# Optimization experiments

Measured on AMD Instinct MI355X. Metric: run time of the kernel, lower is better.

## Reference

```python
import jax, jax.numpy as jnp
import numpy as np

B, S, D, H = 4, 1024, 1024, 16
HD = D // H
EPS = 1e-5


def _layernorm(x, g, b):
    m = jnp.mean(x, axis=-1, keepdims=True)
    v = jnp.mean((x - m) ** 2, axis=-1, keepdims=True)
    return (x - m) * jax.lax.rsqrt(v + EPS) * g + b


def setup_inputs() -> dict:
    key = jax.random.key(0)
    ks = jax.random.split(key, 8)
    sc = 1.0 / np.sqrt(D)
    return {
        "x": jax.random.normal(ks[0], (B, S, D), dtype=jnp.float32),
        "seq_len": jax.random.randint(ks[1], (B,), 1, S + 1, dtype=jnp.int32),
        "Wq": jax.random.normal(ks[2], (D, D), dtype=jnp.float32) * sc,
        "bq": jnp.zeros((D,), dtype=jnp.float32),
        "Wk": jax.random.normal(ks[3], (D, D), dtype=jnp.float32) * sc,
        "bk": jnp.zeros((D,), dtype=jnp.float32),
        "Wv": jax.random.normal(ks[4], (D, D), dtype=jnp.float32) * sc,
        "bv": jnp.zeros((D,), dtype=jnp.float32),
        "ln_g": jnp.ones((HD,), dtype=jnp.float32),
        "ln_b": jnp.zeros((HD,), dtype=jnp.float32),
    }


def reference(x, seq_len, Wq, bq, Wk, bk, Wv, bv, ln_g, ln_b):
    # Faithful quirk: k and v are projections of the ALREADY projected q.
    q = x @ Wq.T + bq                      # [B,S,D]
    k = q @ Wk.T + bk
    v = q @ Wv.T + bv
    # [B,S,D] -> [B,H,S,HD]
    def split_heads(t):
        return t.reshape(B, S, H, HD).transpose(0, 2, 1, 3)
    q, k, v = split_heads(q), split_heads(k), split_heads(v)
    # shared per-head LayerNorm over head_dim
    q = _layernorm(q, ln_g, ln_b)
    k = _layernorm(k, ln_g, ln_b)
    v = _layernorm(v, ln_g, ln_b)
    # raw scores (no temperature scaling in the original; temperature=1.0 unused)
    scores = jnp.einsum("bhqd,bhkd->bhqk", q, k)
    # encoder_mask: multiplicative validity mask on key positions, repeated per head
    mask = (jnp.arange(S)[None, :] < seq_len[:, None]).astype(scores.dtype)  # [B,S]
    scores = scores * mask[:, None, None, :]
    attn = jax.nn.softmax(scores, axis=-1)
    # dropout is identity at inference
    out = jnp.einsum("bhqk,bhkd->bhqd", attn, v)
    return out.transpose(0, 2, 1, 3).reshape(B, S, D)
```

## Files before the change

### kernel.cpp

```cpp
#include <hip/hip_runtime.h>

#define B_  4
#define S_  1024
#define D_  1024
#define H_  16
#define HD_ 64
#define EPS_ 1e-5f

typedef _Float16 f16x8 __attribute__((ext_vector_type(8)));
typedef _Float16 f16x4 __attribute__((ext_vector_type(4)));
typedef __bf16 bf16x8 __attribute__((ext_vector_type(8)));
typedef float  f32x4  __attribute__((ext_vector_type(4)));
typedef unsigned short ushort8v __attribute__((ext_vector_type(8)));

static __device__ __forceinline__ unsigned short f2bf(float f) {
  union { float f; unsigned u; } v; v.f = f;
  unsigned r = v.u + 0x7fffu + ((v.u >> 16) & 1u);
  return (unsigned short)(r >> 16);
}
static __device__ __forceinline__ float bf2f(unsigned short u) {
  union { unsigned u; float f; } v; v.u = ((unsigned)u) << 16;
  return v.f;
}

#define GLD16(gp, lp) __builtin_amdgcn_global_load_lds( \
    (const __attribute__((address_space(1))) void*)(gp), \
    (__attribute__((address_space(3))) void*)(lp), 16, 0, 0)

__global__ __launch_bounds__(256) void cvt_all(
    const float* __restrict__ x,  _Float16* __restrict__ xh,
    const float* __restrict__ Wq, _Float16* __restrict__ wqh,
    const float* __restrict__ Wk, _Float16* __restrict__ wkh,
    const float* __restrict__ Wv, _Float16* __restrict__ wvh) {
  int bid = blockIdx.x;
  const float* src; _Float16* dst; int base;
  if (bid < 4096)      { src = x;  dst = xh;  base = bid; }
  else if (bid < 5120) { src = Wq; dst = wqh; base = bid - 4096; }
  else if (bid < 6144) { src = Wk; dst = wkh; base = bid - 5120; }
  else                 { src = Wv; dst = wvh; base = bid - 6144; }
  int i = base * 1024 + threadIdx.x * 4;
  float4 f = *(const float4*)(src + i);
  f16x4 h;
  h.x = (_Float16)f.x; h.y = (_Float16)f.y; h.z = (_Float16)f.z; h.w = (_Float16)f.w;
  *(f16x4*)(dst + i) = h;
}

__global__ __launch_bounds__(256, 2) void gemm_bt_bias(
    const _Float16* __restrict__ A,
    const _Float16* __restrict__ B0, const float* __restrict__ bias0,
    _Float16* __restrict__ C0,
    const _Float16* __restrict__ B1, const float* __restrict__ bias1,
    _Float16* __restrict__ C1,
    int M, int N, int K)
{
  const _Float16* Bm = blockIdx.z ? B1 : B0;
  const float* bias  = blockIdx.z ? bias1 : bias0;
  _Float16* C        = blockIdx.z ? C1 : C0;

  __shared__ _Float16 As[128 * 32];
  __shared__ _Float16 Bs[64 * 32];

  int tid  = threadIdx.x;
  int lane = tid & 63;
  int wave = tid >> 6;
  int wm = wave >> 1, wn = wave & 1;
  int qd = lane >> 4, l15 = lane & 15;

  long row0 = (long)blockIdx.y * 128;
  long col0 = (long)blockIdx.x * 64;

  int r_a = tid >> 2;
  int c_a = (tid & 3) * 8;

  f32x4 acc[4][2] = {};

  for (int kk = 0; kk < K; kk += 32) {
    GLD16(A  + (row0 + r_a) * K + kk + c_a,      As + tid * 8);
    GLD16(A  + (row0 + 64 + r_a) * K + kk + c_a, As + 2048 + tid * 8);
    GLD16(Bm + (col0 + r_a) * K + kk + c_a,      Bs + tid * 8);
    __syncthreads();

    f16x8 af[4], bfr[2];
    for (int t = 0; t < 4; t++)
      af[t]  = *(const f16x8*)(As + (wm * 64 + t * 16 + l15) * 32 + qd * 8);
    for (int j = 0; j < 2; j++)
      bfr[j] = *(const f16x8*)(Bs + (wn * 32 + j * 16 + l15) * 32 + qd * 8);
    for (int i = 0; i < 4; i++)
      for (int j = 0; j < 2; j++)
        acc[i][j] = __builtin_amdgcn_mfma_f32_16x16x32_f16(af[i], bfr[j], acc[i][j], 0, 0, 0);
    __syncthreads();
  }

  for (int i = 0; i < 4; i++) {
    long row = row0 + wm * 64 + i * 16 + qd * 4;
    for (int j = 0; j < 2; j++) {
      long col = col0 + wn * 32 + j * 16 + l15;
      float bv = bias[col];
      for (int r = 0; r < 4; r++)
        C[(row + r) * N + col] = (_Float16)(acc[i][j][r] + bv);
    }
  }
}

__global__ __launch_bounds__(256, 2) void ln_qkv(
    const _Float16* __restrict__ qh,
    const _Float16* __restrict__ kh,
    const _Float16* __restrict__ vh,
    const float* __restrict__ ln_g, const float* __restrict__ ln_b,
    _Float16* __restrict__ Qn,
    _Float16* __restrict__ Kn,
    unsigned short* __restrict__ Vt)
{
  __shared__ unsigned short Vls[256][68];
  int tid = threadIdx.x;
  int s0 = blockIdx.x * 256;
  int h = blockIdx.y, b = blockIdx.z;
  long bh = (long)b * H_ + h;
  long s = s0 + tid;
  long inbase  = ((long)b * S_ + s) * D_ + (long)h * HD_;
  long outbase = (bh * S_ + s) * HD_;

  f16x8 rw[8];
  {
    for (int i = 0; i < 8; i++) rw[i] = *(const f16x8*)(qh + inbase + i * 8);
    float sum = 0.f, sq = 0.f;
    for (int i = 0; i < 8; i++)
      for (int j = 0; j < 8; j++) { float xv = (float)rw[i][j]; sum += xv; sq = fmaf(xv, xv, sq); }
    float m = sum * (1.f / 64.f);
    float inv = rsqrtf(sq * (1.f / 64.f) - m * m + EPS_);
    for (int i = 0; i < 8; i++) {
      f16x8 o;
      for (int j = 0; j < 8; j++)
        o[j] = (_Float16)(((float)rw[i][j] - m) * inv * ln_g[i * 8 + j] + ln_b[i * 8 + j]);
      *(f16x8*)(Qn + outbase + i * 8) = o;
    }
  }
  {
    for (int i = 0; i < 8; i++) rw[i] = *(const f16x8*)(kh + inbase + i * 8);
    float sum = 0.f, sq = 0.f;
    for (int i = 0; i < 8; i++)
      for (int j = 0; j < 8; j++) { float xv = (float)rw[i][j]; sum += xv; sq = fmaf(xv, xv, sq); }
    float m = sum * (1.f / 64.f);
    float inv = rsqrtf(sq * (1.f / 64.f) - m * m + EPS_);
    for (int i = 0; i < 8; i++) {
      f16x8 o;
      for (int j = 0; j < 8; j++)
        o[j] = (_Float16)(((float)rw[i][j] - m) * inv * ln_g[i * 8 + j] + ln_b[i * 8 + j]);
      *(f16x8*)(Kn + outbase + i * 8) = o;
    }
  }
  {
    for (int i = 0; i < 8; i++) rw[i] = *(const f16x8*)(vh + inbase + i * 8);
    float sum = 0.f, sq = 0.f;
    for (int i = 0; i < 8; i++)
      for (int j = 0; j < 8; j++) { float xv = (float)rw[i][j]; sum += xv; sq = fmaf(xv, xv, sq); }
    float m = sum * (1.f / 64.f);
    float inv = rsqrtf(sq * (1.f / 64.f) - m * m + EPS_);
    for (int i = 0; i < 8; i++)
      for (int j = 0; j < 8; j++)
        Vls[tid][i * 8 + j] = f2bf(((float)rw[i][j] - m) * inv * ln_g[i * 8 + j] + ln_b[i * 8 + j]);
  }
  __syncthreads();
  int d = tid >> 2, sc = tid & 3;
  long vbase = (bh * HD_ + d) * S_ + s0 + sc * 64;
  for (int j0 = 0; j0 < 64; j0 += 8) {
    ushort8v w;
    for (int jj = 0; jj < 8; jj++) w[jj] = Vls[sc * 64 + j0 + jj][d];
    *(ushort8v*)(Vt + vbase + j0) = w;
  }
}

__global__ __launch_bounds__(256, 2) void attn(
    const _Float16* __restrict__ Qn,
    const _Float16* __restrict__ Kn,
    const unsigned short* __restrict__ Vt,
    const int* __restrict__ seq_len,
    float* __restrict__ out)
{
  __shared__ _Float16 Ks[2][64 * 32];
  __shared__ unsigned short Vts[2][64 * 32];
  __shared__ unsigned short Ps[4][16 * 72];

  int tid = threadIdx.x, lane = tid & 63, wave = tid >> 6;
  int qd = lane >> 4, l15 = lane & 15;
  int q0 = blockIdx.x * 64;
  int h = blockIdx.y, b = blockIdx.z;
  long bh = (long)b * H_ + h;
  int len = seq_len[b];

  int skey = tid >> 2;
  int schunk = (tid & 3) * 8;

  f16x8 qf[2];
  {
    const _Float16* qp = Qn + (bh * S_ + q0 + wave * 16 + l15) * HD_;
    qf[0] = *(const f16x8*)(qp + qd * 8);
    qf[1] = *(const f16x8*)(qp + 32 + qd * 8);
  }

  f32x4 o[4] = {};
  float den[4] = {0.f, 0.f, 0.f, 0.f};

  for (int kt = 0; kt < S_ / 64; kt++) {
    GLD16(Kn + (bh * S_ + kt * 64 + skey) * HD_ + schunk,      &Ks[0][0] + tid * 8);
    GLD16(Kn + (bh * S_ + kt * 64 + skey) * HD_ + 32 + schunk, &Ks[1][0] + tid * 8);
    GLD16(Vt + (bh * HD_ + skey) * S_ + kt * 64 + schunk,      &Vts[0][0] + tid * 8);
    GLD16(Vt + (bh * HD_ + skey) * S_ + kt * 64 + 32 + schunk, &Vts[1][0] + tid * 8);
    __syncthreads();

    f32x4 sacc[4] = {};
    for (int tn = 0; tn < 4; tn++) {
      f16x8 kf0 = *(const f16x8*)(&Ks[0][0] + (tn * 16 + l15) * 32 + qd * 8);
      f16x8 kf1 = *(const f16x8*)(&Ks[1][0] + (tn * 16 + l15) * 32 + qd * 8);
      sacc[tn] = __builtin_amdgcn_mfma_f32_16x16x32_f16(qf[0], kf0, sacc[tn], 0, 0, 0);
      sacc[tn] = __builtin_amdgcn_mfma_f32_16x16x32_f16(qf[1], kf1, sacc[tn], 0, 0, 0);
    }

    for (int tn = 0; tn < 4; tn++) {
      int kg = kt * 64 + tn * 16 + l15;
      for (int r = 0; r < 4; r++) {
        float sv = (kg < len) ? sacc[tn][r] : 0.0f;
        float p = __expf(sv);
        unsigned short pb = f2bf(p);
        den[r] += bf2f(pb);
        Ps[wave][(qd * 4 + r) * 72 + tn * 16 + l15] = pb;
      }
    }

    bf16x8 pf0 = *(const bf16x8*)(&Ps[wave][l15 * 72 + qd * 8]);
    bf16x8 pf1 = *(const bf16x8*)(&Ps[wave][l15 * 72 + 32 + qd * 8]);
    for (int t = 0; t < 4; t++) {
      bf16x8 vf0 = *(const bf16x8*)(&Vts[0][0] + (t * 16 + l15) * 32 + qd * 8);
      bf16x8 vf1 = *(const bf16x8*)(&Vts[1][0] + (t * 16 + l15) * 32 + qd * 8);
      o[t] = __builtin_amdgcn_mfma_f32_16x16x32_bf16(pf0, vf0, o[t], 0, 0, 0);
      o[t] = __builtin_amdgcn_mfma_f32_16x16x32_bf16(pf1, vf1, o[t], 0, 0, 0);
    }
    __syncthreads();
  }

  for (int r = 0; r < 4; r++)
    for (int off = 1; off < 16; off <<= 1)
      den[r] += __shfl_xor(den[r], off, 64);

  for (int t = 0; t < 4; t++) {
    for (int r = 0; r < 4; r++) {
      long s = q0 + wave * 16 + qd * 4 + r;
      long dcol = (long)h * HD_ + t * 16 + l15;
      out[((long)b * S_ + s) * D_ + dcol] = o[t][r] / den[r];
    }
  }
}

extern "C" void kernel_launch(void* const* d_in, const int* in_sizes, int n_in,
                              void* d_out, int out_size, void* d_ws, size_t ws_size,
                              hipStream_t stream) {
  const float* x     = (const float*)d_in[0];
  const int*  seq    = (const int*)d_in[1];
  const float* Wq    = (const float*)d_in[2];
  const float* bq    = (const float*)d_in[3];
  const float* Wk    = (const float*)d_in[4];
  const float* bk    = (const float*)d_in[5];
  const float* Wv    = (const float*)d_in[6];
  const float* bv    = (const float*)d_in[7];
  const float* ln_g  = (const float*)d_in[8];
  const float* ln_b  = (const float*)d_in[9];
  float* out = (float*)d_out;

  char* ws = (char*)d_ws;
  _Float16* xh  = (_Float16*)(ws);
  _Float16* wqh = (_Float16*)(ws + (8l  << 20));
  _Float16* wkh = (_Float16*)(ws + (10l << 20));
  _Float16* wvh = (_Float16*)(ws + (12l << 20));
  _Float16* qh  = (_Float16*)(ws + (16l << 20));
  _Float16* kh  = (_Float16*)(ws + (24l << 20));
  _Float16* vh  = (_Float16*)(ws + (32l << 20));
  _Float16* Qn  = (_Float16*)(ws + (40l << 20));
  _Float16* Kn  = (_Float16*)(ws + (48l << 20));
  unsigned short* Vt = (unsigned short*)(ws + (56l << 20));

  cvt_all<<<7168, 256, 0, stream>>>(x, xh, Wq, wqh, Wk, wkh, Wv, wvh);

  dim3 g1(D_ / 64, (B_ * S_) / 128, 1);
  gemm_bt_bias<<<g1, 256, 0, stream>>>(xh, wqh, bq, qh, wqh, bq, qh,
                                       B_ * S_, D_, D_);
  dim3 g2(D_ / 64, (B_ * S_) / 128, 2);
  gemm_bt_bias<<<g2, 256, 0, stream>>>(qh, wkh, bk, kh, wvh, bv, vh,
                                       B_ * S_, D_, D_);

  dim3 g3(S_ / 256, H_, B_);
  ln_qkv<<<g3, 256, 0, stream>>>(qh, kh, vh, ln_g, ln_b, Qn, Kn, Vt);

  dim3 g4(S_ / 64, H_, B_);
  attn<<<g4, 256, 0, stream>>>(Qn, Kn, Vt, seq, out);
}
```

Baseline: 194.8 us.

## Skip masked key tiles via precomputed V tail sums; double query rows per wave

Masked keys get score 0 and so weight exp(0)=1. Their contribution to the output is therefore the sum of their V rows, and to the denominator it is S-len. The ln_qkv kernel now accumulates per-head tail sums of V with atomics, and the attention loop only runs over ceil(len/64) key tiles. Each wave also handles 32 query rows instead of 16, halving the block count and reusing each K/V tile load across twice the rows. This adds atomics and a zeroing pass, and the tail sum uses bf16-rounded V in fp32 instead of exact per-tile accumulation.

```diff
diff --git a/kernel.cpp b/kernel.cpp
--- a/kernel.cpp
+++ b/kernel.cpp
@@ -31,8 +31,14 @@
     const float* __restrict__ x,  _Float16* __restrict__ xh,
     const float* __restrict__ Wq, _Float16* __restrict__ wqh,
     const float* __restrict__ Wk, _Float16* __restrict__ wkh,
-    const float* __restrict__ Wv, _Float16* __restrict__ wvh) {
+    const float* __restrict__ Wv, _Float16* __restrict__ wvh,
+    float* __restrict__ Vtail) {
   int bid = blockIdx.x;
+  if (bid >= 7168) {
+    int i = (bid - 7168) * 1024 + threadIdx.x * 4;
+    *(float4*)(Vtail + i) = make_float4(0.f, 0.f, 0.f, 0.f);
+    return;
+  }
   const float* src; _Float16* dst; int base;
   if (bid < 4096)      { src = x;  dst = xh;  base = bid; }
   else if (bid < 5120) { src = Wq; dst = wqh; base = bid - 4096; }
@@ -107,9 +113,11 @@
     const _Float16* __restrict__ kh,
     const _Float16* __restrict__ vh,
     const float* __restrict__ ln_g, const float* __restrict__ ln_b,
+    const int* __restrict__ seq_len,
     _Float16* __restrict__ Qn,
     _Float16* __restrict__ Kn,
-    unsigned short* __restrict__ Vt)
+    unsigned short* __restrict__ Vt,
+    float* __restrict__ Vtail)
 {
   __shared__ unsigned short Vls[256][68];
   int tid = threadIdx.x;
@@ -162,93 +170,120 @@
   }
   __syncthreads();
   int d = tid >> 2, sc = tid & 3;
+  int len = seq_len[b];
   long vbase = (bh * HD_ + d) * S_ + s0 + sc * 64;
+  float tsum = 0.f;
   for (int j0 = 0; j0 < 64; j0 += 8) {
     ushort8v w;
-    for (int jj = 0; jj < 8; jj++) w[jj] = Vls[sc * 64 + j0 + jj][d];
+    for (int jj = 0; jj < 8; jj++) {
+      unsigned short ub = Vls[sc * 64 + j0 + jj][d];
+      w[jj] = ub;
+      if (s0 + sc * 64 + j0 + jj >= len) tsum += bf2f(ub);
+    }
     *(ushort8v*)(Vt + vbase + j0) = w;
   }
+  if (s0 + sc * 64 + 64 > len)
+    atomicAdd(&Vtail[bh * HD_ + d], tsum);
 }
 
 __global__ __launch_bounds__(256, 2) void attn(
     const _Float16* __restrict__ Qn,
     const _Float16* __restrict__ Kn,
     const unsigned short* __restrict__ Vt,
+    const float* __restrict__ Vtail,
     const int* __restrict__ seq_len,
     float* __restrict__ out)
 {
   __shared__ _Float16 Ks[2][64 * 32];
   __shared__ unsigned short Vts[2][64 * 32];
-  __shared__ unsigned short Ps[4][16 * 72];
+  __shared__ unsigned short Ps[4][32 * 72];
 
   int tid = threadIdx.x, lane = tid & 63, wave = tid >> 6;
   int qd = lane >> 4, l15 = lane & 15;
-  int q0 = blockIdx.x * 64;
+  int q0 = blockIdx.x * 128;
   int h = blockIdx.y, b = blockIdx.z;
   long bh = (long)b * H_ + h;
   int len = seq_len[b];
+  int ntile = (len + 63) >> 6;
 
   int skey = tid >> 2;
   int schunk = (tid & 3) * 8;
 
-  f16x8 qf[2];
-  {
-    const _Float16* qp = Qn + (bh * S_ + q0 + wave * 16 + l15) * HD_;
-    qf[0] = *(const f16x8*)(qp + qd * 8);
-    qf[1] = *(const f16x8*)(qp + 32 + qd * 8);
-  }
-
-  f32x4 o[4] = {};
-  float den[4] = {0.f, 0.f, 0.f, 0.f};
-
-  for (int kt = 0; kt < S_ / 64; kt++) {
+  f16x8 qf[2][2];
+  for (int mt = 0; mt < 2; mt++) {
+    const _Float16* qp = Qn + (bh * S_ + q0 + wave * 32 + mt * 16 + l15) * HD_;
+    qf[mt][0] = *(const f16x8*)(qp + qd * 8);
+    qf[mt][1] = *(const f16x8*)(qp + 32 + qd * 8);
+  }
+
+  f32x4 o[2][4] = {};
+  float den[2][4] = {{0.f,0.f,0.f,0.f},{0.f,0.f,0.f,0.f}};
+
+  for (int kt = 0; kt < ntile; kt++) {
     GLD16(Kn + (bh * S_ + kt * 64 + skey) * HD_ + schunk,      &Ks[0][0] + tid * 8);
     GLD16(Kn + (bh * S_ + kt * 64 + skey) * HD_ + 32 + schunk, &Ks[1][0] + tid * 8);
     GLD16(Vt + (bh * HD_ + skey) * S_ + kt * 64 + schunk,      &Vts[0][0] + tid * 8);
     GLD16(Vt + (bh * HD_ + skey) * S_ + kt * 64 + 32 + schunk, &Vts[1][0] + tid * 8);
     __syncthreads();
 
-    f32x4 sacc[4] = {};
+    f32x4 sacc[2][4] = {};
     for (int tn = 0; tn < 4; tn++) {
       f16x8 kf0 = *(const f16x8*)(&Ks[0][0] + (tn * 16 + l15) * 32 + qd * 8);
       f16x8 kf1 = *(const f16x8*)(&Ks[1][0] + (tn * 16 + l15) * 32 + qd * 8);
-      sacc[tn] = __builtin_amdgcn_mfma_f32_16x16x32_f16(qf[0], kf0, sacc[tn], 0, 0, 0);
-      sacc[tn] = __builtin_amdgcn_mfma_f32_16x16x32_f16(qf[1], kf1, sacc[tn], 0, 0, 0);
-    }
-
-    for (int tn = 0; tn < 4; tn++) {
-      int kg = kt * 64 + tn * 16 + l15;
-      for (int r = 0; r < 4; r++) {
-        float sv = (kg < len) ? sacc[tn][r] : 0.0f;
-        float p = __expf(sv);
-        unsigned short pb = f2bf(p);
-        den[r] += bf2f(pb);
-        Ps[wave][(qd * 4 + r) * 72 + tn * 16 + l15] = pb;
+      for (int mt = 0; mt < 2; mt++) {
+        sacc[mt][tn] = __builtin_amdgcn_mfma_f32_16x16x32_f16(qf[mt][0], kf0, sacc[mt][tn], 0, 0, 0);
+        sacc[mt][tn] = __builtin_amdgcn_mfma_f32_16x16x32_f16(qf[mt][1], kf1, sacc[mt][tn], 0, 0, 0);
       }
     }
 
-    bf16x8 pf0 = *(const bf16x8*)(&Ps[wave][l15 * 72 + qd * 8]);
-    bf16x8 pf1 = *(const bf16x8*)(&Ps[wave][l15 * 72 + 32 + qd * 8]);
+    for (int mt = 0; mt < 2; mt++)
+      for (int tn = 0; tn < 4; tn++) {
+        int kg = kt * 64 + tn * 16 + l15;
+        for (int r = 0; r < 4; r++) {
+          float p = (kg < len) ? __expf(sacc[mt][tn][r]) : 0.f;
+          unsigned short pb = f2bf(p);
+          den[mt][r] += bf2f(pb);
+          Ps[wave][(mt * 16 + qd * 4 + r) * 72 + tn * 16 + l15] = pb;
+        }
+      }
+
+    bf16x8 pf[2][2];
+    for (int mt = 0; mt < 2; mt++) {
+      pf[mt][0] = *(const bf16x8*)(&Ps[wave][(mt * 16 + l15) * 72 + qd * 8]);
+      pf[mt][1] = *(const bf16x8*)(&Ps[wave][(mt * 16 + l15) * 72 + 32 + qd * 8]);
+    }
     for (int t = 0; t < 4; t++) {
       bf16x8 vf0 = *(const bf16x8*)(&Vts[0][0] + (t * 16 + l15) * 32 + qd * 8);
       bf16x8 vf1 = *(const bf16x8*)(&Vts[1][0] + (t * 16 + l15) * 32 + qd * 8);
-      o[t] = __builtin_amdgcn_mfma_f32_16x16x32_bf16(pf0, vf0, o[t], 0, 0, 0);
-      o[t] = __builtin_amdgcn_mfma_f32_16x16x32_bf16(pf1, vf1, o[t], 0, 0, 0);
+      for (int mt = 0; mt < 2; mt++) {
+        o[mt][t] = __builtin_amdgcn_mfma_f32_16x16x32_bf16(pf[mt][0], vf0, o[mt][t], 0, 0, 0);
+        o[mt][t] = __builtin_amdgcn_mfma_f32_16x16x32_bf16(pf[mt][1], vf1, o[mt][t], 0, 0, 0);
+      }
     }
     __syncthreads();
   }
 
-  for (int r = 0; r < 4; r++)
-    for (int off = 1; off < 16; off <<= 1)
-      den[r] += __shfl_xor(den[r], off, 64);
-
-  for (int t = 0; t < 4; t++) {
+  float tv[4];
+  for (int t = 0; t < 4; t++) tv[t] = Vtail[bh * HD_ + t * 16 + l15];
+  for (int mt = 0; mt < 2; mt++)
+    for (int t = 0; t < 4; t++)
+      for (int r = 0; r < 4; r++) o[mt][t][r] += tv[t];
+
+  float tden = (float)(S_ - len);
+  for (int mt = 0; mt < 2; mt++)
     for (int r = 0; r < 4; r++) {
-      long s = q0 + wave * 16 + qd * 4 + r;
-      long dcol = (long)h * HD_ + t * 16 + l15;
-      out[((long)b * S_ + s) * D_ + dcol] = o[t][r] / den[r];
-    }
-  }
+      for (int off = 1; off < 16; off <<= 1)
+        den[mt][r] += __shfl_xor(den[mt][r], off, 64);
+      den[mt][r] += tden;
+    }
+
+  for (int mt = 0; mt < 2; mt++)
+    for (int t = 0; t < 4; t++)
+      for (int r = 0; r < 4; r++) {
+        long s = q0 + wave * 32 + mt * 16 + qd * 4 + r;
+        long dcol = (long)h * HD_ + t * 16 + l15;
+        out[((long)b * S_ + s) * D_ + dcol] = o[mt][t][r] / den[mt][r];
+      }
 }
 
 extern "C" void kernel_launch(void* const* d_in, const int* in_sizes, int n_in,
@@ -271,6 +306,7 @@
   _Float16* wqh = (_Float16*)(ws + (8l  << 20));
   _Float16* wkh = (_Float16*)(ws + (10l << 20));
   _Float16* wvh = (_Float16*)(ws + (12l << 20));
+  float*    Vtail = (float*)(ws + (14l << 20));
   _Float16* qh  = (_Float16*)(ws + (16l << 20));
   _Float16* kh  = (_Float16*)(ws + (24l << 20));
   _Float16* vh  = (_Float16*)(ws + (32l << 20));
@@ -278,7 +314,7 @@
   _Float16* Kn  = (_Float16*)(ws + (48l << 20));
   unsigned short* Vt = (unsigned short*)(ws + (56l << 20));
 
-  cvt_all<<<7168, 256, 0, stream>>>(x, xh, Wq, wqh, Wk, wkh, Wv, wvh);
+  cvt_all<<<7172, 256, 0, stream>>>(x, xh, Wq, wqh, Wk, wkh, Wv, wvh, Vtail);
 
   dim3 g1(D_ / 64, (B_ * S_) / 128, 1);
   gemm_bt_bias<<<g1, 256, 0, stream>>>(xh, wqh, bq, qh, wqh, bq, qh,
@@ -288,8 +324,8 @@
                                        B_ * S_, D_, D_);
 
   dim3 g3(S_ / 256, H_, B_);
-  ln_qkv<<<g3, 256, 0, stream>>>(qh, kh, vh, ln_g, ln_b, Qn, Kn, Vt);
-
-  dim3 g4(S_ / 64, H_, B_);
-  attn<<<g4, 256, 0, stream>>>(Qn, Kn, Vt, seq, out);
-}
+  ln_qkv<<<g3, 256, 0, stream>>>(qh, kh, vh, ln_g, ln_b, seq, Qn, Kn, Vt, Vtail);
+
+  dim3 g4(S_ / 128, H_, B_);
+  attn<<<g4, 256, 0, stream>>>(Qn, Kn, Vt, Vtail, seq, out);
+}
```

Result: no change. 191.6 us (-1.6%).
